# Performance work log

Measured on AMD Instinct MI355X. Metric: run time of the kernel, lower is better.

The kernel has to match this reference:

```python
import jax, jax.numpy as jnp
import numpy as np

B, T = 64, 2048          # batch, encoder max steps
E, A, P = 256, 128, 128  # embedding_dim, attention_dim, prenet_dim
R, D, H = 1024, 1024, 256  # attention_rnn_dim, decoder_rnn_dim, hidden_dim
F, K = 32, 31            # location n_filters, kernel_size
PAD = (K - 1) // 2
NEG_INF = -1e30  # stands in for -inf; softmax-safe in fp32/bf16


def lstm_cell(x, h, c, W_ih, W_hh, b_ih, b_hh):
    # torch.nn.LSTMCell gate order: i, f, g, o
    gates = x @ W_ih.T + h @ W_hh.T + (b_ih + b_hh)
    i, f, g, o = jnp.split(gates, 4, axis=-1)
    c2 = jax.nn.sigmoid(f) * c + jax.nn.sigmoid(i) * jnp.tanh(g)
    h2 = jax.nn.sigmoid(o) * jnp.tanh(c2)
    return h2, c2


def setup_inputs() -> dict:
    key = jax.random.key(0)
    ks = jax.random.split(key, 30)
    n = jax.random.normal
    s = 0.02  # weight scale
    inp = {
        "last_frame": n(ks[0], (B, P)),
        "att_h": n(ks[1], (B, R)) * 0.1,
        "att_c": n(ks[2], (B, R)) * 0.1,
        "att_w": jax.random.uniform(ks[3], (B, T)) / T,
        "att_w_cum": jax.random.uniform(ks[4], (B, T)),
        "att_ctx": n(ks[5], (B, E)) * 0.1,
        "dec_h": n(ks[6], (B, D)) * 0.1,
        "dec_c": n(ks[7], (B, D)) * 0.1,
        "memory": n(ks[8], (B, T, E)),
        "processed_memory": n(ks[9], (B, T, A)) * 0.1,
        # attention LSTMCell (input = embedding_dim + prenet_dim = 384)
        "W_ih_a": n(ks[10], (4 * R, E + P)) * s,
        "W_hh_a": n(ks[11], (4 * R, R)) * s,
        "b_ih_a": n(ks[12], (4 * R,)) * s,
        "b_hh_a": n(ks[13], (4 * R,)) * s,
        # attention layer
        "W_q": n(ks[14], (A, R)) * s,
        "W_v": n(ks[15], (1, A)) * s,
        "W_loc": n(ks[16], (F, 2, K)) * s,   # Conv1d(2 -> F, k=31), no bias
        "W_lfc": n(ks[17], (A, F)) * s,
        # decoder LSTMCell (input = attention_rnn_dim + embedding_dim = 1280)
        "W_ih_d": n(ks[18], (4 * D, R + E)) * s,
        "W_hh_d": n(ks[19], (4 * D, D)) * s,
        "b_ih_d": n(ks[20], (4 * D,)) * s,
        "b_hh_d": n(ks[21], (4 * D,)) * s,
        # output heads
        "W_proj": n(ks[22], (H, D + E)) * s,
        "b_proj": n(ks[23], (H,)) * s,
        "W_gate": n(ks[24], (1, D + E)) * s,
        "b_gate": n(ks[25], (1,)) * s,
        "mask": jax.random.randint(ks[26], (B, T), 0, 2).astype(bool),
    }
    return inp


def reference(last_frame, att_h, att_c, att_w, att_w_cum, att_ctx, dec_h, dec_c,
              memory, processed_memory,
              W_ih_a, W_hh_a, b_ih_a, b_hh_a,
              W_q, W_v, W_loc, W_lfc,
              W_ih_d, W_hh_d, b_ih_d, b_hh_d,
              W_proj, b_proj, W_gate, b_gate, mask):
    # ---- attention RNN step (dropout = identity at eval) ----
    attention_in = jnp.concatenate([last_frame, att_ctx], axis=-1)  # [B, P+E]
    ah, ac = lstm_cell(attention_in, att_h, att_c, W_ih_a, W_hh_a, b_ih_a, b_hh_a)

    # ---- location-sensitive attention ----
    aw_cat = jnp.stack([att_w, att_w_cum], axis=1)  # [B, 2, T]
    loc = jax.lax.conv_general_dilated(
        aw_cat, W_loc, window_strides=(1,), padding=[(PAD, PAD)],
        dimension_numbers=('NCH', 'OIH', 'NCH'))  # [B, F, T]
    loc = jnp.einsum('bft,af->bta', loc, W_lfc)    # LocationLayer fc, [B, T, A]

    pq = (ah @ W_q.T)[:, None, :]                   # processed query [B, 1, A]
    energies = jnp.tanh(pq + processed_memory + loc) @ W_v[0]  # [B, T]
    energies = jnp.where(mask, NEG_INF, energies)
    weights = jax.nn.softmax(energies, axis=1)      # [B, T]
    ctx = jnp.einsum('bt,bte->be', weights, memory)  # [B, E]

    # ---- decoder RNN step ----
    decoder_in = jnp.concatenate([ah, ctx], axis=-1)  # [B, R+E]
    dh, dc = lstm_cell(decoder_in, dec_h, dec_c, W_ih_d, W_hh_d, b_ih_d, b_hh_d)

    dhac = jnp.concatenate([dh, ctx], axis=1)         # [B, D+E]
    decoder_output = dhac @ W_proj.T + b_proj          # [B, H]
    stop_prediction = dhac @ W_gate.T + b_gate         # [B, 1]
    return decoder_output, stop_prediction, weights[:, None, :]  # [B, 1, T]
```

## Files before the change

kernel.cpp:

```cpp
#include <hip/hip_runtime.h>
#include <stdint.h>

typedef unsigned short u16;
typedef __attribute__((ext_vector_type(8))) u16 u16x8;
typedef __attribute__((ext_vector_type(8))) __bf16 bf16x8;
typedef __attribute__((ext_vector_type(4))) float f32x4;

#define L2E 1.4426950408889634f

__device__ __forceinline__ float bf2f(u16 u) {
  union { unsigned i; float f; } v; v.i = ((unsigned)u) << 16; return v.f;
}
__device__ __forceinline__ u16 f2bf_rne(float f) {
  union { float f; unsigned u; } v; v.f = f;
  const unsigned r = v.u + 0x7FFFu + ((v.u >> 16) & 1u);
  return (u16)(r >> 16);
}
__device__ __forceinline__ bf16x8 ldb(const u16* p) {
  u16x8 v = *reinterpret_cast<const u16x8*>(p);
  return __builtin_bit_cast(bf16x8, v);
}
__device__ __forceinline__ void split8t(const float* p, bf16x8& h, bf16x8& l) {
  const float4 v0 = *reinterpret_cast<const float4*>(p);
  const float4 v1 = *reinterpret_cast<const float4*>(p + 4);
  const float f[8] = {v0.x, v0.y, v0.z, v0.w, v1.x, v1.y, v1.z, v1.w};
  u16x8 hu, lu;
#pragma unroll
  for (int i = 0; i < 8; ++i) {
    union { float f; unsigned u; } a; a.f = f[i];
    hu[i] = (u16)(a.u >> 16);
    union { float f; unsigned u; } hf; hf.u = a.u & 0xFFFF0000u;
    union { float f; unsigned u; } lo; lo.f = f[i] - hf.f;
    lu[i] = (u16)(lo.u >> 16);
  }
  h = __builtin_bit_cast(bf16x8, hu);
  l = __builtin_bit_cast(bf16x8, lu);
}
__device__ __forceinline__ f32x4 mfma16(bf16x8 a, bf16x8 b, f32x4 c) {
  return __builtin_amdgcn_mfma_f32_16x16x32_bf16(a, b, c, 0, 0, 0);
}
__device__ __forceinline__ float sigm(float x) {
  return 1.0f / (1.0f + exp2f(-L2E * x));
}
__device__ __forceinline__ float tanh_(float x) {
  return 1.0f - 2.0f / (1.0f + exp2f(2.0f * L2E * x));
}

__global__ __launch_bounds__(128) void k0_prep(
    const float* __restrict__ Wloc, const float* __restrict__ Wlfc,
    u16* __restrict__ w2b)
{
  const int k = blockIdx.x, a = threadIdx.x;
  float v = 0.0f;
  if (k < 62) {
    const int c = (k >= 31) ? 1 : 0, dk = k - c * 31;
    for (int f = 0; f < 32; ++f)
      v += Wlfc[a * 32 + f] * Wloc[f * 62 + c * 31 + dk];
  }
  w2b[a * 64 + k] = f2bf_rne(v);
}

#define KSA 8
__global__ __launch_bounds__(256) void k1_gemm(
    const float* __restrict__ lf, const float* __restrict__ actx,
    const float* __restrict__ ah_in,
    const float* __restrict__ Wih, const float* __restrict__ Whh,
    float* __restrict__ gates)
{
  const int tid = threadIdx.x;
  const int g = tid >> 6, lane = tid & 63, quad = lane >> 4, l16 = lane & 15;
  const int jb = blockIdx.x * 16, ks = blockIdx.y;
  const int n = g * 1024 + jb + l16;
  const int s0 = (ks * 44) / KSA, s1 = ((ks + 1) * 44) / KSA;
  f32x4 acc[4] = {{0,0,0,0},{0,0,0,0},{0,0,0,0},{0,0,0,0}};
  for (int s = s0; s < s1; ++s) {
    const int kb = s * 32, k = kb + quad * 8;
    const float* bp = (k < 384) ? (Wih + n * 384 + k) : (Whh + n * 1024 + (k - 384));
    bf16x8 b_h, b_l; split8t(bp, b_h, b_l);
#pragma unroll
    for (int mt = 0; mt < 4; ++mt) {
      const int mA = mt * 16 + l16;
      const float* ap;
      if (k < 128)      ap = lf    + mA * 128  + k;
      else if (k < 384) ap = actx  + mA * 256  + (k - 128);
      else              ap = ah_in + mA * 1024 + (k - 384);
      bf16x8 a_h, a_l; split8t(ap, a_h, a_l);
      acc[mt] = mfma16(a_h, b_h, acc[mt]);
      acc[mt] = mfma16(a_h, b_l, acc[mt]);
      acc[mt] = mfma16(a_l, b_h, acc[mt]);
    }
  }
#pragma unroll
  for (int mt = 0; mt < 4; ++mt)
#pragma unroll
    for (int r = 0; r < 4; ++r)
      atomicAdd(&gates[(mt * 16 + quad * 4 + r) * 4096 + n], acc[mt][r]);
}

__global__ __launch_bounds__(256) void k1_epi(
    const float* __restrict__ gates, const float* __restrict__ ac_in,
    const float* __restrict__ bih, const float* __restrict__ bhh,
    float* __restrict__ ah_f, u16* __restrict__ xd)
{
  const int lin = blockIdx.x * 256 + threadIdx.x;
  const int m = lin >> 10, j = lin & 1023;
  const float pi = gates[m * 4096 + j]        + bih[j]        + bhh[j];
  const float pf = gates[m * 4096 + 1024 + j] + bih[1024 + j] + bhh[1024 + j];
  const float pg = gates[m * 4096 + 2048 + j] + bih[2048 + j] + bhh[2048 + j];
  const float po = gates[m * 4096 + 3072 + j] + bih[3072 + j] + bhh[3072 + j];
  const float c2 = sigm(pf) * ac_in[m * 1024 + j] + sigm(pi) * tanh_(pg);
  const float h2 = sigm(po) * tanh_(c2);
  ah_f[m * 1024 + j] = h2;
  xd[m * 1280 + j]   = f2bf_rne(h2);
}

__global__ __launch_bounds__(256) void k2a_pq(
    const float* __restrict__ ah_f, const float* __restrict__ Wq, float* __restrict__ pq)
{
  const int lane = threadIdx.x & 63;
  const int wid = blockIdx.x * 4 + (threadIdx.x >> 6);
  const int a = wid & 127, bg = wid >> 7;
  float s[4] = {0, 0, 0, 0};
  for (int k = lane; k < 1024; k += 64) {
    const float wq = Wq[a * 1024 + k];
#pragma unroll
    for (int i = 0; i < 4; ++i) s[i] += wq * ah_f[(bg * 4 + i) * 1024 + k];
  }
#pragma unroll
  for (int i = 0; i < 4; ++i) {
    float v = s[i];
    for (int off = 1; off < 64; off <<= 1) v += __shfl_xor(v, off, 64);
    if (lane == 0) pq[(bg * 4 + i) * 128 + a] = v;
  }
}

__global__ __launch_bounds__(256) void k2_energy(
    const float* __restrict__ aw, const float* __restrict__ awc,
    const float* __restrict__ pm, const float* __restrict__ Wv,
    const float* __restrict__ pq, const u16* __restrict__ w2b,
    const int* __restrict__ msk, float* __restrict__ e_g)
{
  __shared__ __align__(16) u16 awin[2][64];
  __shared__ __align__(16) u16 pms[32 * 128];
  __shared__ __align__(16) u16 w2s[128 * 64];
  __shared__ float wvs[128];
  __shared__ float pqs[128];
  __shared__ float es[32];
  const int b = blockIdx.y, t0 = blockIdx.x * 32, tid = threadIdx.x;

  if (tid < 128) {
    const int c = tid >> 6, ii = tid & 63;
    const int t = t0 - 15 + ii;
    float v = 0.0f;
    if (ii < 62 && t >= 0 && t < 2048) v = (c ? awc : aw)[b * 2048 + t];
    awin[c][ii] = f2bf_rne(v);
    wvs[tid] = Wv[tid];
    pqs[tid] = pq[b * 128 + tid];
  }
  if (tid < 32) es[tid] = 0.0f;
  {
    const float* src = pm + (size_t)b * 262144 + (size_t)t0 * 128;
    const int i = tid * 16;
#pragma unroll
    for (int q = 0; q < 4; ++q) {
      const float4 v = *reinterpret_cast<const float4*>(&src[i + q * 4]);
      pms[i + q * 4 + 0] = f2bf_rne(v.x);
      pms[i + q * 4 + 1] = f2bf_rne(v.y);
      pms[i + q * 4 + 2] = f2bf_rne(v.z);
      pms[i + q * 4 + 3] = f2bf_rne(v.w);
    }
  }
  {
    const int i = tid * 32;
#pragma unroll
    for (int q = 0; q < 4; ++q)
      *reinterpret_cast<u16x8*>(&w2s[i + q * 8]) = *reinterpret_cast<const u16x8*>(&w2b[i + q * 8]);
  }
  __syncthreads();

  const int w = tid >> 6, lane = tid & 63, quad = lane >> 4, l16 = lane & 15;
  const int mt = w & 1, ng = w >> 1;
  f32x4 acc[4] = {{0,0,0,0},{0,0,0,0},{0,0,0,0},{0,0,0,0}};
#pragma unroll
  for (int ksx = 0; ksx < 2; ++ksx) {
    bf16x8 af;
    const int m = mt * 16 + l16;
#pragma unroll
    for (int jj = 0; jj < 8; ++jj) {
      const int k = ksx * 32 + quad * 8 + jj;
      u16 v = 0;
      if (k < 62) { const int c = (k >= 31) ? 1 : 0; const int dk = k - c * 31; v = awin[c][m + dk]; }
      af[jj] = __builtin_bit_cast(__bf16, v);
    }
#pragma unroll
    for (int p = 0; p < 4; ++p) {
      const int a = (ng * 4 + p) * 16 + l16;
      bf16x8 bfr = *reinterpret_cast<const bf16x8*>(&w2s[a * 64 + ksx * 32 + quad * 8]);
      acc[p] = mfma16(af, bfr, acc[p]);
    }
  }
#pragma unroll
  for (int r = 0; r < 4; ++r) {
    const int tl = mt * 16 + quad * 4 + r;
    float part = 0.0f;
#pragma unroll
    for (int p = 0; p < 4; ++p) {
      const int a = (ng * 4 + p) * 16 + l16;
      const float x = pqs[a] + bf2f(pms[tl * 128 + a]) + acc[p][r];
      part += wvs[a] * tanh_(x);
    }
    part += __shfl_xor(part, 1, 64);
    part += __shfl_xor(part, 2, 64);
    part += __shfl_xor(part, 4, 64);
    part += __shfl_xor(part, 8, 64);
    if (l16 == 0) atomicAdd(&es[tl], part);
  }
  __syncthreads();
  if (tid < 32) {
    const int t = t0 + tid;
    e_g[b * 2048 + t] = msk[b * 2048 + t] ? -1e30f : es[tid];
  }
}

__global__ __launch_bounds__(256) void k3a_softmax(
    const float* __restrict__ e_g, float* __restrict__ w_f, float* __restrict__ out_w)
{
  const int b = blockIdx.x, tid = threadIdx.x;
  __shared__ float red[4];
  float v[8];
  float mx = -3.0e38f;
#pragma unroll
  for (int i = 0; i < 8; ++i) { v[i] = e_g[b * 2048 + tid + i * 256]; mx = fmaxf(mx, v[i]); }
  for (int off = 1; off < 64; off <<= 1) mx = fmaxf(mx, __shfl_xor(mx, off, 64));
  if ((tid & 63) == 0) red[tid >> 6] = mx;
  __syncthreads();
  mx = fmaxf(fmaxf(red[0], red[1]), fmaxf(red[2], red[3]));
  float ex[8], s = 0.0f;
#pragma unroll
  for (int i = 0; i < 8; ++i) { ex[i] = exp2f((v[i] - mx) * L2E); s += ex[i]; }
  for (int off = 1; off < 64; off <<= 1) s += __shfl_xor(s, off, 64);
  __syncthreads();
  if ((tid & 63) == 0) red[tid >> 6] = s;
  __syncthreads();
  const float rs = 1.0f / (red[0] + red[1] + red[2] + red[3]);
#pragma unroll
  for (int i = 0; i < 8; ++i) {
    const int t = tid + i * 256;
    const float wv = ex[i] * rs;
    w_f[b * 2048 + t]   = wv;
    out_w[b * 2048 + t] = wv;
  }
}

__global__ __launch_bounds__(256) void k3b_ctx(
    const float* __restrict__ w_f, const float* __restrict__ mem, float* __restrict__ ctx)
{
  const int b = blockIdx.y, tc = blockIdx.x, tid = threadIdx.x;
  const int w = tid >> 6, lane = tid & 63;
  __shared__ float wsm[256];
  __shared__ float red[4][256];
  wsm[tid] = w_f[b * 2048 + tc * 256 + tid];
  __syncthreads();
  const float* mp = mem + (size_t)b * 524288 + ((size_t)tc * 256 + w * 64) * 256 + lane * 4;
  f32x4 acc = {0, 0, 0, 0};
#pragma unroll 4
  for (int t = 0; t < 64; ++t) {
    const float wt = wsm[w * 64 + t];
    const float4 v = *reinterpret_cast<const float4*>(mp + (size_t)t * 256);
    acc[0] += wt * v.x; acc[1] += wt * v.y; acc[2] += wt * v.z; acc[3] += wt * v.w;
  }
#pragma unroll
  for (int i = 0; i < 4; ++i) red[w][lane * 4 + i] = acc[i];
  __syncthreads();
  const float s = red[0][tid] + red[1][tid] + red[2][tid] + red[3][tid];
  atomicAdd(&ctx[b * 256 + tid], s);
}

__global__ __launch_bounds__(256) void k3c_cvt(
    const float* __restrict__ ctx, u16* __restrict__ xd, u16* __restrict__ dhac)
{
  const int b = blockIdx.x, e = threadIdx.x;
  const u16 v = f2bf_rne(ctx[b * 256 + e]);
  xd[b * 1280 + 1024 + e]   = v;
  dhac[b * 1280 + 1024 + e] = v;
}

__global__ __launch_bounds__(256) void k4_gemm(
    const u16* __restrict__ xd, const float* __restrict__ dh_in,
    const float* __restrict__ Wih, const float* __restrict__ Whh,
    float* __restrict__ gates)
{
  const int tid = threadIdx.x;
  const int g = tid >> 6, lane = tid & 63, quad = lane >> 4, l16 = lane & 15;
  const int jb = blockIdx.x * 16, ks = blockIdx.y;
  const int n = g * 1024 + jb + l16;
  const int kb0 = ks * 256, kb1 = kb0 + 256;
  f32x4 acc[4] = {{0,0,0,0},{0,0,0,0},{0,0,0,0},{0,0,0,0}};
  for (int kb = kb0; kb < kb1; kb += 32) {
    const int k = kb + quad * 8;
    const float* bp = (k < 1280) ? (Wih + n * 1280 + k) : (Whh + n * 1024 + (k - 1280));
    bf16x8 b_h, b_l; split8t(bp, b_h, b_l);
    if (k < 1280) {
#pragma unroll
      for (int mt = 0; mt < 4; ++mt) {
        bf16x8 a_h = ldb(xd + (mt * 16 + l16) * 1280 + k);
        acc[mt] = mfma16(a_h, b_h, acc[mt]);
        acc[mt] = mfma16(a_h, b_l, acc[mt]);
      }
    } else {
#pragma unroll
      for (int mt = 0; mt < 4; ++mt) {
        bf16x8 a_h, a_l; split8t(dh_in + (mt * 16 + l16) * 1024 + (k - 1280), a_h, a_l);
        acc[mt] = mfma16(a_h, b_h, acc[mt]);
        acc[mt] = mfma16(a_h, b_l, acc[mt]);
        acc[mt] = mfma16(a_l, b_h, acc[mt]);
      }
    }
  }
#pragma unroll
  for (int mt = 0; mt < 4; ++mt)
#pragma unroll
    for (int r = 0; r < 4; ++r)
      atomicAdd(&gates[(mt * 16 + quad * 4 + r) * 4096 + n], acc[mt][r]);
}

__global__ __launch_bounds__(256) void k4_epi(
    const float* __restrict__ gates, const float* __restrict__ dc_in,
    const float* __restrict__ bih, const float* __restrict__ bhh,
    u16* __restrict__ dhac)
{
  const int lin = blockIdx.x * 256 + threadIdx.x;
  const int m = lin >> 10, j = lin & 1023;
  const float pi = gates[m * 4096 + j]        + bih[j]        + bhh[j];
  const float pf = gates[m * 4096 + 1024 + j] + bih[1024 + j] + bhh[1024 + j];
  const float pg = gates[m * 4096 + 2048 + j] + bih[2048 + j] + bhh[2048 + j];
  const float po = gates[m * 4096 + 3072 + j] + bih[3072 + j] + bhh[3072 + j];
  const float c2 = sigm(pf) * dc_in[m * 1024 + j] + sigm(pi) * tanh_(pg);
  const float h2 = sigm(po) * tanh_(c2);
  dhac[m * 1280 + j] = f2bf_rne(h2);
}

__global__ __launch_bounds__(256) void k5_gemm(
    const u16* __restrict__ dhac, const float* __restrict__ Wp,
    float* __restrict__ proj)
{
  const int tid = threadIdx.x;
  const int w = tid >> 6, lane = tid & 63, quad = lane >> 4, l16 = lane & 15;
  const int n = blockIdx.x * 64 + w * 16 + l16, ks = blockIdx.y;
  const int kb0 = ks * 64;
  f32x4 acc[4] = {{0,0,0,0},{0,0,0,0},{0,0,0,0},{0,0,0,0}};
#pragma unroll
  for (int kb = kb0; kb < kb0 + 64; kb += 32) {
    const int k = kb + quad * 8;
    bf16x8 b_h, b_l; split8t(Wp + n * 1280 + k, b_h, b_l);
#pragma unroll
    for (int mt = 0; mt < 4; ++mt) {
      bf16x8 af = ldb(dhac + (mt * 16 + l16) * 1280 + k);
      acc[mt] = mfma16(af, b_h, acc[mt]);
      acc[mt] = mfma16(af, b_l, acc[mt]);
    }
  }
#pragma unroll
  for (int mt = 0; mt < 4; ++mt)
#pragma unroll
    for (int r = 0; r < 4; ++r)
      atomicAdd(&proj[(mt * 16 + quad * 4 + r) * 256 + n], acc[mt][r]);
}

__global__ __launch_bounds__(256) void k5_epi(
    const float* __restrict__ proj, const float* __restrict__ bp,
    const u16* __restrict__ dhac, const float* __restrict__ Wg,
    const float* __restrict__ bg, float* __restrict__ out)
{
  const int tid = threadIdx.x;
  if (blockIdx.x < 64) {
    const int m = blockIdx.x;
    out[m * 256 + tid] = proj[m * 256 + tid] + bp[tid];
  } else {
    const int w = tid >> 6, lane = tid & 63;
    const int bb = (blockIdx.x - 64) * 4 + w;
    float s = 0.0f;
    for (int k = lane; k < 1280; k += 64) s += bf2f(dhac[bb * 1280 + k]) * Wg[k];
    for (int off = 1; off < 64; off <<= 1) s += __shfl_xor(s, off, 64);
    if (lane == 0) out[16384 + bb] = s + bg[0];
  }
}

extern "C" void kernel_launch(void* const* d_in, const int* in_sizes, int n_in,
                              void* d_out, int out_size, void* d_ws, size_t ws_size,
                              hipStream_t stream)
{
  const float* lf    = (const float*)d_in[0];
  const float* ah0   = (const float*)d_in[1];
  const float* ac0   = (const float*)d_in[2];
  const float* aw    = (const float*)d_in[3];
  const float* awc   = (const float*)d_in[4];
  const float* actx  = (const float*)d_in[5];
  const float* dh0   = (const float*)d_in[6];
  const float* dc0   = (const float*)d_in[7];
  const float* mem   = (const float*)d_in[8];
  const float* pm    = (const float*)d_in[9];
  const float* Wih_a = (const float*)d_in[10];
  const float* Whh_a = (const float*)d_in[11];
  const float* bih_a = (const float*)d_in[12];
  const float* bhh_a = (const float*)d_in[13];
  const float* Wq    = (const float*)d_in[14];
  const float* Wv    = (const float*)d_in[15];
  const float* Wloc  = (const float*)d_in[16];
  const float* Wlfc  = (const float*)d_in[17];
  const float* Wih_d = (const float*)d_in[18];
  const float* Whh_d = (const float*)d_in[19];
  const float* bih_d = (const float*)d_in[20];
  const float* bhh_d = (const float*)d_in[21];
  const float* Wp    = (const float*)d_in[22];
  const float* bp    = (const float*)d_in[23];
  const float* Wg    = (const float*)d_in[24];
  const float* bg    = (const float*)d_in[25];
  const int* msk     = (const int*)d_in[26];

  float* wsf     = (float*)d_ws;
  float* gates_a = wsf;
  float* gates_d = wsf + 262144;
  float* proj    = wsf + 524288;
  float* ctx     = wsf + 540672;
  float* ah_f    = wsf + 557056;
  float* pq      = wsf + 622592;
  float* e_g     = wsf + 630784;
  float* w_f     = wsf + 761856;
  u16*  xd       = (u16*)(wsf + 892928);
  u16*  dhac     = xd + 81920;
  u16*  w2b      = dhac + 81920;

  float* out   = (float*)d_out;
  float* out_w = out + 16448;

  hipMemsetAsync(d_ws, 0, 557056 * sizeof(float), stream);

  k0_prep    <<<64, 128, 0, stream>>>(Wloc, Wlfc, w2b);
  k1_gemm    <<<dim3(64, KSA), 256, 0, stream>>>(lf, actx, ah0, Wih_a, Whh_a, gates_a);
  k1_epi     <<<256, 256, 0, stream>>>(gates_a, ac0, bih_a, bhh_a, ah_f, xd);
  k2a_pq     <<<512, 256, 0, stream>>>(ah_f, Wq, pq);
  k2_energy  <<<dim3(64, 64), 256, 0, stream>>>(aw, awc, pm, Wv, pq, w2b, msk, e_g);
  k3a_softmax<<<64, 256, 0, stream>>>(e_g, w_f, out_w);
  k3b_ctx    <<<dim3(8, 64), 256, 0, stream>>>(w_f, mem, ctx);
  k3c_cvt    <<<64, 256, 0, stream>>>(ctx, xd, dhac);
  k4_gemm    <<<dim3(64, 9), 256, 0, stream>>>(xd, dh0, Wih_d, Whh_d, gates_d);
  k4_epi     <<<256, 256, 0, stream>>>(gates_d, dc0, bih_d, bhh_d, dhac);
  k5_gemm    <<<dim3(4, 20), 256, 0, stream>>>(dhac, Wp, proj);
  k5_epi     <<<80, 256, 0, stream>>>(proj, bp, dhac, Wg, bg, out);
}
```

Measured before the change: 400.3 us.

## Replace atomic split-K accumulation with partial buffers and fuse softmax into ctx

The split-K GEMMs and the ctx reduction now write per-slice partial buffers, and the epilogues sum those slices instead of using atomicAdd. This removes the workspace memset and the atomic contention. Softmax is recomputed redundantly inside each ctx block, which drops one launch and the w_f round trip. k2a_pq is rewritten with float4 loads, and k4 converts ctx to bf16 on the fly with 8 K-slices of 9 steps each. The cost is more workspace traffic: 8 partial gate buffers of 1 MB each are written and then read back.

```diff
diff --git a/kernel.cpp b/kernel.cpp
--- a/kernel.cpp
+++ b/kernel.cpp
@@ -36,6 +36,15 @@
   h = __builtin_bit_cast(bf16x8, hu);
   l = __builtin_bit_cast(bf16x8, lu);
 }
+__device__ __forceinline__ bf16x8 cvt8_rne(const float* p) {
+  const float4 v0 = *reinterpret_cast<const float4*>(p);
+  const float4 v1 = *reinterpret_cast<const float4*>(p + 4);
+  const float f[8] = {v0.x, v0.y, v0.z, v0.w, v1.x, v1.y, v1.z, v1.w};
+  u16x8 u;
+#pragma unroll
+  for (int i = 0; i < 8; ++i) u[i] = f2bf_rne(f[i]);
+  return __builtin_bit_cast(bf16x8, u);
+}
 __device__ __forceinline__ f32x4 mfma16(bf16x8 a, bf16x8 b, f32x4 c) {
   return __builtin_amdgcn_mfma_f32_16x16x32_bf16(a, b, c, 0, 0, 0);
 }
@@ -60,21 +69,20 @@
   w2b[a * 64 + k] = f2bf_rne(v);
 }
 
-#define KSA 8
 __global__ __launch_bounds__(256) void k1_gemm(
     const float* __restrict__ lf, const float* __restrict__ actx,
     const float* __restrict__ ah_in,
     const float* __restrict__ Wih, const float* __restrict__ Whh,
-    float* __restrict__ gates)
+    float* __restrict__ gpart)
 {
   const int tid = threadIdx.x;
   const int g = tid >> 6, lane = tid & 63, quad = lane >> 4, l16 = lane & 15;
   const int jb = blockIdx.x * 16, ks = blockIdx.y;
   const int n = g * 1024 + jb + l16;
-  const int s0 = (ks * 44) / KSA, s1 = ((ks + 1) * 44) / KSA;
+  const int s0 = (ks * 44) / 8, s1 = ((ks + 1) * 44) / 8;
   f32x4 acc[4] = {{0,0,0,0},{0,0,0,0},{0,0,0,0},{0,0,0,0}};
   for (int s = s0; s < s1; ++s) {
-    const int kb = s * 32, k = kb + quad * 8;
+    const int k = s * 32 + quad * 8;
     const float* bp = (k < 384) ? (Wih + n * 384 + k) : (Whh + n * 1024 + (k - 384));
     bf16x8 b_h, b_l; split8t(bp, b_h, b_l);
 #pragma unroll
@@ -90,47 +98,61 @@
       acc[mt] = mfma16(a_l, b_h, acc[mt]);
     }
   }
+  float* dst = gpart + (size_t)ks * 262144;
 #pragma unroll
   for (int mt = 0; mt < 4; ++mt)
 #pragma unroll
     for (int r = 0; r < 4; ++r)
-      atomicAdd(&gates[(mt * 16 + quad * 4 + r) * 4096 + n], acc[mt][r]);
+      dst[(mt * 16 + quad * 4 + r) * 4096 + n] = acc[mt][r];
 }
 
 __global__ __launch_bounds__(256) void k1_epi(
-    const float* __restrict__ gates, const float* __restrict__ ac_in,
+    const float* __restrict__ gpart, const float* __restrict__ ac_in,
     const float* __restrict__ bih, const float* __restrict__ bhh,
     float* __restrict__ ah_f, u16* __restrict__ xd)
 {
   const int lin = blockIdx.x * 256 + threadIdx.x;
   const int m = lin >> 10, j = lin & 1023;
-  const float pi = gates[m * 4096 + j]        + bih[j]        + bhh[j];
-  const float pf = gates[m * 4096 + 1024 + j] + bih[1024 + j] + bhh[1024 + j];
-  const float pg = gates[m * 4096 + 2048 + j] + bih[2048 + j] + bhh[2048 + j];
-  const float po = gates[m * 4096 + 3072 + j] + bih[3072 + j] + bhh[3072 + j];
+  float p4[4] = {0, 0, 0, 0};
+  for (int ks = 0; ks < 8; ++ks) {
+    const float* gp = gpart + (size_t)ks * 262144 + m * 4096 + j;
+    p4[0] += gp[0];
+    p4[1] += gp[1024];
+    p4[2] += gp[2048];
+    p4[3] += gp[3072];
+  }
+  const float pi = p4[0] + bih[j]        + bhh[j];
+  const float pf = p4[1] + bih[1024 + j] + bhh[1024 + j];
+  const float pg = p4[2] + bih[2048 + j] + bhh[2048 + j];
+  const float po = p4[3] + bih[3072 + j] + bhh[3072 + j];
   const float c2 = sigm(pf) * ac_in[m * 1024 + j] + sigm(pi) * tanh_(pg);
   const float h2 = sigm(po) * tanh_(c2);
   ah_f[m * 1024 + j] = h2;
-  xd[m * 1280 + j]   = f2bf_rne(h2);
+  xd[m * 1024 + j]   = f2bf_rne(h2);
 }
 
 __global__ __launch_bounds__(256) void k2a_pq(
-    const float* __restrict__ ah_f, const float* __restrict__ Wq, float* __restrict__ pq)
-{
-  const int lane = threadIdx.x & 63;
-  const int wid = blockIdx.x * 4 + (threadIdx.x >> 6);
-  const int a = wid & 127, bg = wid >> 7;
-  float s[4] = {0, 0, 0, 0};
-  for (int k = lane; k < 1024; k += 64) {
-    const float wq = Wq[a * 1024 + k];
-#pragma unroll
-    for (int i = 0; i < 4; ++i) s[i] += wq * ah_f[(bg * 4 + i) * 1024 + k];
-  }
+    const float* __restrict__ ah_f, const float* __restrict__ Wq,
+    float* __restrict__ pq)
+{
+  const int b = blockIdx.y, ch = blockIdx.x;
+  const int w = threadIdx.x >> 6, lane = threadIdx.x & 63;
+  const float4* xp = reinterpret_cast<const float4*>(ah_f + b * 1024);
+  float4 x[4];
+#pragma unroll
+  for (int it = 0; it < 4; ++it) x[it] = xp[it * 64 + lane];
 #pragma unroll
   for (int i = 0; i < 4; ++i) {
-    float v = s[i];
-    for (int off = 1; off < 64; off <<= 1) v += __shfl_xor(v, off, 64);
-    if (lane == 0) pq[(bg * 4 + i) * 128 + a] = v;
+    const int a = ch * 16 + w * 4 + i;
+    const float4* wp = reinterpret_cast<const float4*>(Wq + a * 1024);
+    float s = 0.0f;
+#pragma unroll
+    for (int it = 0; it < 4; ++it) {
+      const float4 q = wp[it * 64 + lane];
+      s += q.x * x[it].x + q.y * x[it].y + q.z * x[it].z + q.w * x[it].w;
+    }
+    for (int off = 1; off < 64; off <<= 1) s += __shfl_xor(s, off, 64);
+    if (lane == 0) pq[b * 128 + a] = s;
   }
 }
 
@@ -222,88 +244,91 @@
   }
 }
 
-__global__ __launch_bounds__(256) void k3a_softmax(
-    const float* __restrict__ e_g, float* __restrict__ w_f, float* __restrict__ out_w)
-{
-  const int b = blockIdx.x, tid = threadIdx.x;
-  __shared__ float red[4];
-  float v[8];
+__global__ __launch_bounds__(256) void k3f_ctx(
+    const float* __restrict__ e_g, const float* __restrict__ mem,
+    float* __restrict__ ctx_p, float* __restrict__ out_w)
+{
+  const int tc = blockIdx.x, b = blockIdx.y, tid = threadIdx.x;
+  const int w = tid >> 6, lane = tid & 63;
+  __shared__ float red4[4];
+  __shared__ float wsm[256];
+  __shared__ float redc[4][256];
+  float v8[8];
   float mx = -3.0e38f;
 #pragma unroll
-  for (int i = 0; i < 8; ++i) { v[i] = e_g[b * 2048 + tid + i * 256]; mx = fmaxf(mx, v[i]); }
+  for (int i = 0; i < 8; ++i) { v8[i] = e_g[b * 2048 + tid + i * 256]; mx = fmaxf(mx, v8[i]); }
   for (int off = 1; off < 64; off <<= 1) mx = fmaxf(mx, __shfl_xor(mx, off, 64));
-  if ((tid & 63) == 0) red[tid >> 6] = mx;
-  __syncthreads();
-  mx = fmaxf(fmaxf(red[0], red[1]), fmaxf(red[2], red[3]));
+  if ((tid & 63) == 0) red4[tid >> 6] = mx;
+  __syncthreads();
+  mx = fmaxf(fmaxf(red4[0], red4[1]), fmaxf(red4[2], red4[3]));
   float ex[8], s = 0.0f;
 #pragma unroll
-  for (int i = 0; i < 8; ++i) { ex[i] = exp2f((v[i] - mx) * L2E); s += ex[i]; }
+  for (int i = 0; i < 8; ++i) { ex[i] = exp2f((v8[i] - mx) * L2E); s += ex[i]; }
   for (int off = 1; off < 64; off <<= 1) s += __shfl_xor(s, off, 64);
   __syncthreads();
-  if ((tid & 63) == 0) red[tid >> 6] = s;
-  __syncthreads();
-  const float rs = 1.0f / (red[0] + red[1] + red[2] + red[3]);
-#pragma unroll
-  for (int i = 0; i < 8; ++i) {
-    const int t = tid + i * 256;
-    const float wv = ex[i] * rs;
-    w_f[b * 2048 + t]   = wv;
-    out_w[b * 2048 + t] = wv;
-  }
-}
-
-__global__ __launch_bounds__(256) void k3b_ctx(
-    const float* __restrict__ w_f, const float* __restrict__ mem, float* __restrict__ ctx)
-{
-  const int b = blockIdx.y, tc = blockIdx.x, tid = threadIdx.x;
-  const int w = tid >> 6, lane = tid & 63;
-  __shared__ float wsm[256];
-  __shared__ float red[4][256];
-  wsm[tid] = w_f[b * 2048 + tc * 256 + tid];
+  if ((tid & 63) == 0) red4[tid >> 6] = s;
+  __syncthreads();
+  const float rs = 1.0f / (red4[0] + red4[1] + red4[2] + red4[3]);
+  float exc = 0.0f;
+#pragma unroll
+  for (int i = 0; i < 8; ++i) if (i == tc) exc = ex[i];
+  const float wv = exc * rs;
+  out_w[b * 2048 + tc * 256 + tid] = wv;
+  wsm[tid] = wv;
   __syncthreads();
   const float* mp = mem + (size_t)b * 524288 + ((size_t)tc * 256 + w * 64) * 256 + lane * 4;
   f32x4 acc = {0, 0, 0, 0};
-#pragma unroll 4
+#pragma unroll 8
   for (int t = 0; t < 64; ++t) {
     const float wt = wsm[w * 64 + t];
     const float4 v = *reinterpret_cast<const float4*>(mp + (size_t)t * 256);
     acc[0] += wt * v.x; acc[1] += wt * v.y; acc[2] += wt * v.z; acc[3] += wt * v.w;
   }
 #pragma unroll
-  for (int i = 0; i < 4; ++i) red[w][lane * 4 + i] = acc[i];
-  __syncthreads();
-  const float s = red[0][tid] + red[1][tid] + red[2][tid] + red[3][tid];
-  atomicAdd(&ctx[b * 256 + tid], s);
-}
-
-__global__ __launch_bounds__(256) void k3c_cvt(
-    const float* __restrict__ ctx, u16* __restrict__ xd, u16* __restrict__ dhac)
+  for (int i = 0; i < 4; ++i) redc[w][lane * 4 + i] = acc[i];
+  __syncthreads();
+  const float s2 = redc[0][tid] + redc[1][tid] + redc[2][tid] + redc[3][tid];
+  ctx_p[tc * 16384 + b * 256 + tid] = s2;
+}
+
+__global__ __launch_bounds__(256) void k3s_sum(
+    const float* __restrict__ ctx_p, float* __restrict__ ctx,
+    u16* __restrict__ dhac)
 {
   const int b = blockIdx.x, e = threadIdx.x;
-  const u16 v = f2bf_rne(ctx[b * 256 + e]);
-  xd[b * 1280 + 1024 + e]   = v;
-  dhac[b * 1280 + 1024 + e] = v;
+  float s = 0.0f;
+#pragma unroll
+  for (int tc = 0; tc < 8; ++tc) s += ctx_p[tc * 16384 + b * 256 + e];
+  ctx[b * 256 + e] = s;
+  dhac[b * 1280 + 1024 + e] = f2bf_rne(s);
 }
 
 __global__ __launch_bounds__(256) void k4_gemm(
-    const u16* __restrict__ xd, const float* __restrict__ dh_in,
+    const u16* __restrict__ xd, const float* __restrict__ ctx,
+    const float* __restrict__ dh_in,
     const float* __restrict__ Wih, const float* __restrict__ Whh,
-    float* __restrict__ gates)
+    float* __restrict__ gpart)
 {
   const int tid = threadIdx.x;
   const int g = tid >> 6, lane = tid & 63, quad = lane >> 4, l16 = lane & 15;
   const int jb = blockIdx.x * 16, ks = blockIdx.y;
   const int n = g * 1024 + jb + l16;
-  const int kb0 = ks * 256, kb1 = kb0 + 256;
   f32x4 acc[4] = {{0,0,0,0},{0,0,0,0},{0,0,0,0},{0,0,0,0}};
-  for (int kb = kb0; kb < kb1; kb += 32) {
-    const int k = kb + quad * 8;
+  for (int s = ks * 9; s < ks * 9 + 9; ++s) {
+    const int k = s * 32 + quad * 8;
     const float* bp = (k < 1280) ? (Wih + n * 1280 + k) : (Whh + n * 1024 + (k - 1280));
     bf16x8 b_h, b_l; split8t(bp, b_h, b_l);
-    if (k < 1280) {
+    if (k < 1024) {
 #pragma unroll
       for (int mt = 0; mt < 4; ++mt) {
-        bf16x8 a_h = ldb(xd + (mt * 16 + l16) * 1280 + k);
+        bf16x8 a_h = ldb(xd + (mt * 16 + l16) * 1024 + k);
+        acc[mt] = mfma16(a_h, b_h, acc[mt]);
+        acc[mt] = mfma16(a_h, b_l, acc[mt]);
+      }
+    } else if (k < 1280) {
+#pragma unroll
+      for (int mt = 0; mt < 4; ++mt) {
+        bf16x8 a_h = cvt8_rne(ctx + (mt * 16 + l16) * 256 + (k - 1024));
         acc[mt] = mfma16(a_h, b_h, acc[mt]);
         acc[mt] = mfma16(a_h, b_l, acc[mt]);
       }
@@ -317,24 +342,33 @@
       }
     }
   }
+  float* dst = gpart + (size_t)ks * 262144;
 #pragma unroll
   for (int mt = 0; mt < 4; ++mt)
 #pragma unroll
     for (int r = 0; r < 4; ++r)
-      atomicAdd(&gates[(mt * 16 + quad * 4 + r) * 4096 + n], acc[mt][r]);
+      dst[(mt * 16 + quad * 4 + r) * 4096 + n] = acc[mt][r];
 }
 
 __global__ __launch_bounds__(256) void k4_epi(
-    const float* __restrict__ gates, const float* __restrict__ dc_in,
+    const float* __restrict__ gpart, const float* __restrict__ dc_in,
     const float* __restrict__ bih, const float* __restrict__ bhh,
     u16* __restrict__ dhac)
 {
   const int lin = blockIdx.x * 256 + threadIdx.x;
   const int m = lin >> 10, j = lin & 1023;
-  const float pi = gates[m * 4096 + j]        + bih[j]        + bhh[j];
-  const float pf = gates[m * 4096 + 1024 + j] + bih[1024 + j] + bhh[1024 + j];
-  const float pg = gates[m * 4096 + 2048 + j] + bih[2048 + j] + bhh[2048 + j];
-  const float po = gates[m * 4096 + 3072 + j] + bih[3072 + j] + bhh[3072 + j];
+  float p4[4] = {0, 0, 0, 0};
+  for (int ks = 0; ks < 8; ++ks) {
+    const float* gp = gpart + (size_t)ks * 262144 + m * 4096 + j;
+    p4[0] += gp[0];
+    p4[1] += gp[1024];
+    p4[2] += gp[2048];
+    p4[3] += gp[3072];
+  }
+  const float pi = p4[0] + bih[j]        + bhh[j];
+  const float pf = p4[1] + bih[1024 + j] + bhh[1024 + j];
+  const float pg = p4[2] + bih[2048 + j] + bhh[2048 + j];
+  const float po = p4[3] + bih[3072 + j] + bhh[3072 + j];
   const float c2 = sigm(pf) * dc_in[m * 1024 + j] + sigm(pi) * tanh_(pg);
   const float h2 = sigm(po) * tanh_(c2);
   dhac[m * 1280 + j] = f2bf_rne(h2);
@@ -342,7 +376,7 @@
 
 __global__ __launch_bounds__(256) void k5_gemm(
     const u16* __restrict__ dhac, const float* __restrict__ Wp,
-    float* __restrict__ proj)
+    float* __restrict__ proj_p)
 {
   const int tid = threadIdx.x;
   const int w = tid >> 6, lane = tid & 63, quad = lane >> 4, l16 = lane & 15;
@@ -360,22 +394,26 @@
       acc[mt] = mfma16(af, b_l, acc[mt]);
     }
   }
+  float* dst = proj_p + (size_t)ks * 16384;
 #pragma unroll
   for (int mt = 0; mt < 4; ++mt)
 #pragma unroll
     for (int r = 0; r < 4; ++r)
-      atomicAdd(&proj[(mt * 16 + quad * 4 + r) * 256 + n], acc[mt][r]);
+      dst[(mt * 16 + quad * 4 + r) * 256 + n] = acc[mt][r];
 }
 
 __global__ __launch_bounds__(256) void k5_epi(
-    const float* __restrict__ proj, const float* __restrict__ bp,
+    const float* __restrict__ proj_p, const float* __restrict__ bp,
     const u16* __restrict__ dhac, const float* __restrict__ Wg,
     const float* __restrict__ bg, float* __restrict__ out)
 {
   const int tid = threadIdx.x;
   if (blockIdx.x < 64) {
     const int m = blockIdx.x;
-    out[m * 256 + tid] = proj[m * 256 + tid] + bp[tid];
+    float s = bp[tid];
+#pragma unroll
+    for (int ks = 0; ks < 20; ++ks) s += proj_p[(size_t)ks * 16384 + m * 256 + tid];
+    out[m * 256 + tid] = s;
   } else {
     const int w = tid >> 6, lane = tid & 63;
     const int bb = (blockIdx.x - 64) * 4 + w;
@@ -390,6 +428,7 @@
                               void* d_out, int out_size, void* d_ws, size_t ws_size,
                               hipStream_t stream)
 {
+  (void)in_sizes; (void)n_in; (void)out_size; (void)ws_size;
   const float* lf    = (const float*)d_in[0];
   const float* ah0   = (const float*)d_in[1];
   const float* ac0   = (const float*)d_in[2];
@@ -419,33 +458,30 @@
   const int* msk     = (const int*)d_in[26];
 
   float* wsf     = (float*)d_ws;
-  float* gates_a = wsf;
-  float* gates_d = wsf + 262144;
-  float* proj    = wsf + 524288;
-  float* ctx     = wsf + 540672;
-  float* ah_f    = wsf + 557056;
-  float* pq      = wsf + 622592;
-  float* e_g     = wsf + 630784;
-  float* w_f     = wsf + 761856;
-  u16*  xd       = (u16*)(wsf + 892928);
-  u16*  dhac     = xd + 81920;
+  float* ga_part = wsf;
+  float* gd_part = wsf + 2097152;
+  float* proj_p  = wsf + 4194304;
+  float* ctx_p   = wsf + 4521984;
+  float* ctx     = wsf + 4653056;
+  float* ah_f    = wsf + 4669440;
+  float* pq      = wsf + 4734976;
+  float* e_g     = wsf + 4743168;
+  u16*  xd       = (u16*)(wsf + 4874240);
+  u16*  dhac     = xd + 65536;
   u16*  w2b      = dhac + 81920;
 
   float* out   = (float*)d_out;
   float* out_w = out + 16448;
 
-  hipMemsetAsync(d_ws, 0, 557056 * sizeof(float), stream);
-
-  k0_prep    <<<64, 128, 0, stream>>>(Wloc, Wlfc, w2b);
-  k1_gemm    <<<dim3(64, KSA), 256, 0, stream>>>(lf, actx, ah0, Wih_a, Whh_a, gates_a);
-  k1_epi     <<<256, 256, 0, stream>>>(gates_a, ac0, bih_a, bhh_a, ah_f, xd);
-  k2a_pq     <<<512, 256, 0, stream>>>(ah_f, Wq, pq);
-  k2_energy  <<<dim3(64, 64), 256, 0, stream>>>(aw, awc, pm, Wv, pq, w2b, msk, e_g);
-  k3a_softmax<<<64, 256, 0, stream>>>(e_g, w_f, out_w);
-  k3b_ctx    <<<dim3(8, 64), 256, 0, stream>>>(w_f, mem, ctx);
-  k3c_cvt    <<<64, 256, 0, stream>>>(ctx, xd, dhac);
-  k4_gemm    <<<dim3(64, 9), 256, 0, stream>>>(xd, dh0, Wih_d, Whh_d, gates_d);
-  k4_epi     <<<256, 256, 0, stream>>>(gates_d, dc0, bih_d, bhh_d, dhac);
-  k5_gemm    <<<dim3(4, 20), 256, 0, stream>>>(dhac, Wp, proj);
-  k5_epi     <<<80, 256, 0, stream>>>(proj, bp, dhac, Wg, bg, out);
-}
+  k0_prep <<<64, 128, 0, stream>>>(Wloc, Wlfc, w2b);
+  k1_gemm <<<dim3(64, 8), 256, 0, stream>>>(lf, actx, ah0, Wih_a, Whh_a, ga_part);
+  k1_epi  <<<256, 256, 0, stream>>>(ga_part, ac0, bih_a, bhh_a, ah_f, xd);
+  k2a_pq  <<<dim3(8, 64), 256, 0, stream>>>(ah_f, Wq, pq);
+  k2_energy<<<dim3(64, 64), 256, 0, stream>>>(aw, awc, pm, Wv, pq, w2b, msk, e_g);
+  k3f_ctx <<<dim3(8, 64), 256, 0, stream>>>(e_g, mem, ctx_p, out_w);
+  k3s_sum <<<64, 256, 0, stream>>>(ctx_p, ctx, dhac);
+  k4_gemm <<<dim3(64, 8), 256, 0, stream>>>(xd, ctx, dh0, Wih_d, Whh_d, gd_part);
+  k4_epi  <<<256, 256, 0, stream>>>(gd_part, dc0, bih_d, bhh_d, dhac);
+  k5_gemm <<<dim3(4, 20), 256, 0, stream>>>(dhac, Wp, proj_p);
+  k5_epi  <<<80, 256, 0, stream>>>(proj_p, bp, dhac, Wg, bg, out);
+}
```

After: 389.1 us. -2.8%, faster.
